# Kernel optimization log

Hardware: AMD Instinct MI355X
Metric: run time of the kernel (lower is better)

## Reference

```python
import jax, jax.numpy as jnp
import numpy as np

ALPHA = 0.25
GAMMA = 2.0
EPS = 1e-4


def calc_iou(a, b):
    # a: [A,4] anchors xyxy, b: [M,4] gt boxes xyxy -> [A,M]
    area = (b[:, 2] - b[:, 0]) * (b[:, 3] - b[:, 1])  # [M]
    iw = jnp.minimum(a[:, 2:3], b[None, :, 2]) - jnp.maximum(a[:, 0:1], b[None, :, 0])
    ih = jnp.minimum(a[:, 3:4], b[None, :, 3]) - jnp.maximum(a[:, 1:2], b[None, :, 1])
    iw = jnp.clip(iw, 0.0)
    ih = jnp.clip(ih, 0.0)
    anchor_area = ((a[:, 2] - a[:, 0]) * (a[:, 3] - a[:, 1]))[:, None]
    ua = jnp.clip(anchor_area + area[None, :] - iw * ih, 1e-8)
    return iw * ih / ua


def setup_inputs() -> dict:
    B, A, K, M = 8, 120000, 80, 32
    key = jax.random.key(0)
    k1, k2, k3, k4, k5, k6, k7 = jax.random.split(key, 7)
    classifications = jax.random.uniform(k1, (B, A, K), dtype=jnp.float32)
    regressions = jax.random.normal(k2, (B, A, 4), dtype=jnp.float32) * 0.1
    # anchors: valid xyxy boxes with positive width/height
    a_xy = jax.random.uniform(k3, (A, 2), minval=0.0, maxval=480.0)
    a_wh = jax.random.uniform(k4, (A, 2), minval=16.0, maxval=128.0)
    anchors = jnp.concatenate([a_xy, a_xy + a_wh], axis=1)[None].astype(jnp.float32)
    # annotations: [B, M, 5] valid gt boxes, labels in [0, K)
    g_xy = jax.random.uniform(k5, (B, M, 2), minval=0.0, maxval=400.0)
    g_wh = jax.random.uniform(k6, (B, M, 2), minval=20.0, maxval=120.0)
    labels = jax.random.randint(k7, (B, M, 1), 0, K).astype(jnp.float32)
    annotations = jnp.concatenate([g_xy, g_xy + g_wh, labels], axis=2).astype(jnp.float32)
    return {"classifications": classifications, "regressions": regressions,
            "anchors": anchors, "annotations": annotations}


def reference(classifications, regressions, anchors, annotations):
    anchor = anchors[0]  # [A,4]
    aw = anchor[:, 2] - anchor[:, 0]
    ah = anchor[:, 3] - anchor[:, 1]
    acx = anchor[:, 0] + 0.5 * aw
    acy = anchor[:, 1] + 0.5 * ah
    reg_scale = jnp.array([0.1, 0.1, 0.2, 0.2], dtype=classifications.dtype)

    def per_item(cls, reg, ann):
        # cls: [A,K], reg: [A,4], ann: [M,5]
        valid = ann[:, 4] != -1.0  # [M] padding mask
        c = jnp.clip(cls, EPS, 1.0 - EPS)
        iou = jnp.where(valid[None, :], calc_iou(anchor, ann[:, :4]), -1.0)  # [A,M]
        iou_max = iou.max(axis=1)
        iou_argmax = iou.argmax(axis=1)
        assigned = ann[iou_argmax]  # [A,5] gather
        pos = iou_max >= 0.5
        neg = iou_max < 0.4
        num_pos = pos.sum().astype(c.dtype)
        # targets: 1 at assigned class for positives, 0 for negatives, -1 = ignore
        onehot = jax.nn.one_hot(assigned[:, 4].astype(jnp.int32), c.shape[1], dtype=c.dtype)
        t = jnp.where(pos[:, None], onehot, jnp.where(neg[:, None], 0.0, -1.0))
        alpha_factor = jnp.where(t == 1.0, ALPHA, 1.0 - ALPHA)
        focal_weight = jnp.where(t == 1.0, 1.0 - c, c)
        bce = -(t * jnp.log(c) + (1.0 - t) * jnp.log(1.0 - c))
        cls_loss = jnp.where(t != -1.0, alpha_factor * focal_weight ** GAMMA * bce, 0.0)
        cls_loss = cls_loss.sum() / jnp.maximum(num_pos, 1.0)
        gw0 = assigned[:, 2] - assigned[:, 0]
        gh0 = assigned[:, 3] - assigned[:, 1]
        gcx = assigned[:, 0] + 0.5 * gw0
        gcy = assigned[:, 1] + 0.5 * gh0
        gw = jnp.maximum(gw0, 1.0)
        gh = jnp.maximum(gh0, 1.0)
        rt = jnp.stack([(gcx - acx) / aw, (gcy - acy) / ah,
                        jnp.log(gw / aw), jnp.log(gh / ah)], axis=1) / reg_scale
        diff = jnp.abs(rt - reg)
        smooth = jnp.where(diff <= 1.0 / 9.0, 0.5 * 9.0 * diff ** 2, diff - 0.5 / 9.0)
        reg_loss = jnp.where(num_pos > 0.0,
                             (smooth * pos[:, None]).sum() / jnp.maximum(num_pos * 4.0, 1.0),
                             0.0)
        return cls_loss, reg_loss

    cls_l, reg_l = jax.vmap(per_item)(classifications, regressions, annotations)
    return cls_l.mean(keepdims=True), reg_l.mean(keepdims=True)
```

## Files before the change

kernel.cpp:

```cpp
#include <hip/hip_runtime.h>

#define NB 8
#define NA 120000
#define NK 80
#define NM 32

#define ALPHA_F 0.25f
#define EPS_F 1e-4f

#define BLK 256
#define BPB ((NA + BLK - 1) / BLK)

__device__ __forceinline__ float clampc(float x) {
    return fminf(fmaxf(x, EPS_F), 1.0f - EPS_F);
}
__device__ __forceinline__ float negl(float c) {
    return (1.0f - ALPHA_F) * c * c * (-__logf(1.0f - c));
}
__device__ __forceinline__ float posl(float c) {
    const float omc = 1.0f - c;
    return ALPHA_F * omc * omc * (-__logf(c));
}
__device__ __forceinline__ float negl4(float4 v) {
    return negl(clampc(v.x)) + negl(clampc(v.y)) + negl(clampc(v.z)) + negl(clampc(v.w));
}

__global__ __launch_bounds__(BLK) void fused_kernel(
    const float* __restrict__ anchors,
    const float* __restrict__ regressions,
    const float* __restrict__ annotations,
    const float* __restrict__ cls,
    float* __restrict__ part)
{
    const int b = blockIdx.x / BPB;
    const int blk = blockIdx.x % BPB;
    const int a0 = blk * BLK;
    const int a = a0 + threadIdx.x;

    __shared__ float ann[NM * 5];
    __shared__ float barea[NM];
    __shared__ int s_ign[BLK];
    __shared__ int s_nign;
    if (threadIdx.x == 0) s_nign = 0;
    if (threadIdx.x < NM * 5) ann[threadIdx.x] = annotations[b * NM * 5 + threadIdx.x];
    __syncthreads();
    if (threadIdx.x < NM) {
        const float* r = &ann[threadIdx.x * 5];
        barea[threadIdx.x] = (r[2] - r[0]) * (r[3] - r[1]);
    }
    __syncthreads();

    float reg_local = 0.0f;
    float pos_local = 0.0f;
    float cls_local = 0.0f;

    if (a < NA) {
        const float4 av = ((const float4*)anchors)[a];
        const float aw = av.z - av.x;
        const float ah = av.w - av.y;
        const float aarea = aw * ah;

        float bi = -1.0f, bu = 1.0f;
        int bm = 0;
        #pragma unroll
        for (int m = 0; m < NM; ++m) {
            const float bx1 = ann[m * 5 + 0];
            const float by1 = ann[m * 5 + 1];
            const float bx2 = ann[m * 5 + 2];
            const float by2 = ann[m * 5 + 3];
            const float lbl = ann[m * 5 + 4];
            const float iw = fmaxf(fminf(av.z, bx2) - fmaxf(av.x, bx1), 0.0f);
            const float ih = fmaxf(fminf(av.w, by2) - fmaxf(av.y, by1), 0.0f);
            float inter = iw * ih;
            float ua = fmaxf(aarea + barea[m] - inter, 1e-8f);
            if (lbl == -1.0f) { inter = -1.0f; ua = 1.0f; }
            if (m == 0 || inter * bu > bi * ua) { bi = inter; bu = ua; bm = m; }
        }

        if (bi >= 0.5f * bu) {
            const int st = (int)ann[bm * 5 + 4];
            const float bx1 = ann[bm * 5 + 0];
            const float by1 = ann[bm * 5 + 1];
            const float bx2 = ann[bm * 5 + 2];
            const float by2 = ann[bm * 5 + 3];
            const float gw0 = bx2 - bx1;
            const float gh0 = by2 - by1;
            const float gcx = bx1 + 0.5f * gw0;
            const float gcy = by1 + 0.5f * gh0;
            const float gw = fmaxf(gw0, 1.0f);
            const float gh = fmaxf(gh0, 1.0f);
            const float acx = av.x + 0.5f * aw;
            const float acy = av.y + 0.5f * ah;
            const float rt0 = ((gcx - acx) / aw) / 0.1f;
            const float rt1 = ((gcy - acy) / ah) / 0.1f;
            const float rt2 = logf(gw / aw) / 0.2f;
            const float rt3 = logf(gh / ah) / 0.2f;
            const float4 rg = ((const float4*)regressions)[b * NA + a];
            float s = 0.0f, d;
            d = fabsf(rt0 - rg.x); s += (d <= 1.0f / 9.0f) ? 4.5f * d * d : d - 0.5f / 9.0f;
            d = fabsf(rt1 - rg.y); s += (d <= 1.0f / 9.0f) ? 4.5f * d * d : d - 0.5f / 9.0f;
            d = fabsf(rt2 - rg.z); s += (d <= 1.0f / 9.0f) ? 4.5f * d * d : d - 0.5f / 9.0f;
            d = fabsf(rt3 - rg.w); s += (d <= 1.0f / 9.0f) ? 4.5f * d * d : d - 0.5f / 9.0f;
            reg_local = s;
            pos_local = 1.0f;
            const float c = clampc(cls[((size_t)b * NA + a) * NK + st]);
            cls_local = posl(c) - negl(c);
        } else if (bi >= 0.4f * bu) {
            const int k = atomicAdd(&s_nign, 1);
            s_ign[k] = threadIdx.x;
        }
    }
    __syncthreads();

    const float4* __restrict__ p = (const float4*)(cls + ((size_t)b * NA + a0) * NK);
    const int n_rows = (a0 + BLK <= NA) ? BLK : (NA - a0);

    if (n_rows == BLK) {
        #pragma unroll
        for (int o = 0; o < 4; ++o) {
            float4 v[5];
            #pragma unroll
            for (int u = 0; u < 5; ++u)
                v[u] = p[(o * 5 + u) * BLK + threadIdx.x];
            #pragma unroll
            for (int u = 0; u < 5; ++u)
                cls_local += negl4(v[u]);
        }
    } else {
        const int n4 = n_rows * 20;
        for (int idx = threadIdx.x; idx < n4; idx += BLK)
            cls_local += negl4(p[idx]);
    }

    const int nign = s_nign;
    if (nign > 0) {
        const int total = nign * 20;
        for (int i = threadIdx.x; i < total; i += BLK) {
            const int e = i / 20;
            const int f = i - e * 20;
            const int r = s_ign[e];
            cls_local -= negl4(p[r * 20 + f]);
        }
    }

    #pragma unroll
    for (int o = 32; o > 0; o >>= 1) {
        cls_local += __shfl_down(cls_local, o, 64);
        reg_local += __shfl_down(reg_local, o, 64);
        pos_local += __shfl_down(pos_local, o, 64);
    }
    __shared__ float wc[BLK / 64], wr[BLK / 64], wp[BLK / 64];
    const int lane = threadIdx.x & 63;
    const int wid = threadIdx.x >> 6;
    if (lane == 0) { wc[wid] = cls_local; wr[wid] = reg_local; wp[wid] = pos_local; }
    __syncthreads();
    if (threadIdx.x == 0) {
        float csum = 0.0f, rsum = 0.0f, psum = 0.0f;
        #pragma unroll
        for (int i = 0; i < BLK / 64; ++i) { csum += wc[i]; rsum += wr[i]; psum += wp[i]; }
        float4 q;
        q.x = csum; q.y = rsum; q.z = psum; q.w = 0.0f;
        ((float4*)part)[blockIdx.x] = q;
    }
}

__global__ __launch_bounds__(256) void finalize_kernel(
    const float* __restrict__ part,
    float* __restrict__ out)
{
    __shared__ float red[3][4];
    float cs_total = 0.0f, rs_total = 0.0f;
    for (int b = 0; b < NB; ++b) {
        float c = 0.0f, r = 0.0f, p = 0.0f;
        for (int i = threadIdx.x; i < BPB; i += 256) {
            const float4 q = ((const float4*)part)[b * BPB + i];
            c += q.x; r += q.y; p += q.z;
        }
        #pragma unroll
        for (int o = 32; o > 0; o >>= 1) {
            c += __shfl_down(c, o, 64);
            r += __shfl_down(r, o, 64);
            p += __shfl_down(p, o, 64);
        }
        const int lane = threadIdx.x & 63;
        const int wid = threadIdx.x >> 6;
        if (lane == 0) { red[0][wid] = c; red[1][wid] = r; red[2][wid] = p; }
        __syncthreads();
        if (threadIdx.x == 0) {
            const float C = red[0][0] + red[0][1] + red[0][2] + red[0][3];
            const float R = red[1][0] + red[1][1] + red[1][2] + red[1][3];
            const float P = red[2][0] + red[2][1] + red[2][2] + red[2][3];
            cs_total += C / fmaxf(P, 1.0f);
            rs_total += (P > 0.0f) ? R / fmaxf(P * 4.0f, 1.0f) : 0.0f;
        }
        __syncthreads();
    }
    if (threadIdx.x == 0) {
        out[0] = cs_total / (float)NB;
        out[1] = rs_total / (float)NB;
    }
}

extern "C" void kernel_launch(void* const* d_in, const int* in_sizes, int n_in,
                              void* d_out, int out_size, void* d_ws, size_t ws_size,
                              hipStream_t stream) {
    const float* cls = (const float*)d_in[0];
    const float* reg = (const float*)d_in[1];
    const float* anc = (const float*)d_in[2];
    const float* ann = (const float*)d_in[3];

    float* part = (float*)d_ws;
    float* out = (float*)d_out;

    fused_kernel<<<NB * BPB, BLK, 0, stream>>>(anc, reg, ann, cls, part);
    finalize_kernel<<<1, 256, 0, stream>>>(part, out);
}
```

Before: 83.54 us.

## Prefetch classification tiles before IoU matching and parallelize finalize per batch

```diff
diff --git a/kernel.cpp b/kernel.cpp
--- a/kernel.cpp
+++ b/kernel.cpp
@@ -10,6 +10,7 @@
 
 #define BLK 256
 #define BPB ((NA + BLK - 1) / BLK)
+
 
 __device__ __forceinline__ float clampc(float x) {
     return fminf(fmaxf(x, EPS_F), 1.0f - EPS_F);
@@ -49,6 +50,19 @@
         barea[threadIdx.x] = (r[2] - r[0]) * (r[3] - r[1]);
     }
     __syncthreads();
+
+    const float4* __restrict__ p = (const float4*)(cls + ((size_t)b * NA + a0) * NK);
+    const float4* __restrict__ q = p + threadIdx.x;
+    const int n_rows = (a0 + BLK <= NA) ? BLK : (NA - a0);
+    const bool full = (n_rows == BLK);
+
+    float4 A[5], B[5];
+    if (full) {
+        #pragma unroll
+        for (int u = 0; u < 5; ++u) A[u] = q[u * BLK];
+        #pragma unroll
+        for (int u = 0; u < 5; ++u) B[u] = q[(5 + u) * BLK];
+    }
 
     float reg_local = 0.0f;
     float pos_local = 0.0f;
@@ -112,20 +126,21 @@
     }
     __syncthreads();
 
-    const float4* __restrict__ p = (const float4*)(cls + ((size_t)b * NA + a0) * NK);
-    const int n_rows = (a0 + BLK <= NA) ? BLK : (NA - a0);
-
-    if (n_rows == BLK) {
-        #pragma unroll
-        for (int o = 0; o < 4; ++o) {
-            float4 v[5];
-            #pragma unroll
-            for (int u = 0; u < 5; ++u)
-                v[u] = p[(o * 5 + u) * BLK + threadIdx.x];
-            #pragma unroll
-            for (int u = 0; u < 5; ++u)
-                cls_local += negl4(v[u]);
-        }
+    if (full) {
+        float s = 0.0f;
+        #pragma unroll
+        for (int u = 0; u < 5; ++u) s += negl4(A[u]);
+        #pragma unroll
+        for (int u = 0; u < 5; ++u) A[u] = q[(10 + u) * BLK];
+        #pragma unroll
+        for (int u = 0; u < 5; ++u) s += negl4(B[u]);
+        #pragma unroll
+        for (int u = 0; u < 5; ++u) B[u] = q[(15 + u) * BLK];
+        #pragma unroll
+        for (int u = 0; u < 5; ++u) s += negl4(A[u]);
+        #pragma unroll
+        for (int u = 0; u < 5; ++u) s += negl4(B[u]);
+        cls_local += s;
     } else {
         const int n4 = n_rows * 20;
         for (int idx = threadIdx.x; idx < n4; idx += BLK)
@@ -158,46 +173,43 @@
         float csum = 0.0f, rsum = 0.0f, psum = 0.0f;
         #pragma unroll
         for (int i = 0; i < BLK / 64; ++i) { csum += wc[i]; rsum += wr[i]; psum += wp[i]; }
-        float4 q;
-        q.x = csum; q.y = rsum; q.z = psum; q.w = 0.0f;
-        ((float4*)part)[blockIdx.x] = q;
-    }
-}
-
-__global__ __launch_bounds__(256) void finalize_kernel(
+        float4 o4;
+        o4.x = csum; o4.y = rsum; o4.z = psum; o4.w = 0.0f;
+        ((float4*)part)[blockIdx.x] = o4;
+    }
+}
+
+__global__ __launch_bounds__(512) void finalize_kernel(
     const float* __restrict__ part,
     float* __restrict__ out)
 {
-    __shared__ float red[3][4];
-    float cs_total = 0.0f, rs_total = 0.0f;
-    for (int b = 0; b < NB; ++b) {
-        float c = 0.0f, r = 0.0f, p = 0.0f;
-        for (int i = threadIdx.x; i < BPB; i += 256) {
-            const float4 q = ((const float4*)part)[b * BPB + i];
-            c += q.x; r += q.y; p += q.z;
-        }
-        #pragma unroll
-        for (int o = 32; o > 0; o >>= 1) {
-            c += __shfl_down(c, o, 64);
-            r += __shfl_down(r, o, 64);
-            p += __shfl_down(p, o, 64);
-        }
-        const int lane = threadIdx.x & 63;
-        const int wid = threadIdx.x >> 6;
-        if (lane == 0) { red[0][wid] = c; red[1][wid] = r; red[2][wid] = p; }
-        __syncthreads();
-        if (threadIdx.x == 0) {
-            const float C = red[0][0] + red[0][1] + red[0][2] + red[0][3];
-            const float R = red[1][0] + red[1][1] + red[1][2] + red[1][3];
-            const float P = red[2][0] + red[2][1] + red[2][2] + red[2][3];
-            cs_total += C / fmaxf(P, 1.0f);
-            rs_total += (P > 0.0f) ? R / fmaxf(P * 4.0f, 1.0f) : 0.0f;
-        }
-        __syncthreads();
-    }
+    __shared__ float redC[NB], redR[NB], redP[NB];
+    const int w = threadIdx.x >> 6;
+    const int lane = threadIdx.x & 63;
+
+    float c = 0.0f, r = 0.0f, p = 0.0f;
+    for (int i = lane; i < BPB; i += 64) {
+        const float4 q = ((const float4*)part)[w * BPB + i];
+        c += q.x; r += q.y; p += q.z;
+    }
+    #pragma unroll
+    for (int o = 32; o > 0; o >>= 1) {
+        c += __shfl_down(c, o, 64);
+        r += __shfl_down(r, o, 64);
+        p += __shfl_down(p, o, 64);
+    }
+    if (lane == 0) { redC[w] = c; redR[w] = r; redP[w] = p; }
+    __syncthreads();
     if (threadIdx.x == 0) {
-        out[0] = cs_total / (float)NB;
-        out[1] = rs_total / (float)NB;
+        float cs = 0.0f, rs = 0.0f;
+        #pragma unroll
+        for (int b = 0; b < NB; ++b) {
+            const float P = redP[b];
+            cs += redC[b] / fmaxf(P, 1.0f);
+            rs += (P > 0.0f) ? redR[b] / fmaxf(P * 4.0f, 1.0f) : 0.0f;
+        }
+        out[0] = cs / (float)NB;
+        out[1] = rs / (float)NB;
     }
 }
 
@@ -213,5 +225,5 @@
     float* out = (float*)d_out;
 
     fused_kernel<<<NB * BPB, BLK, 0, stream>>>(anc, reg, ann, cls, part);
-    finalize_kernel<<<1, 256, 0, stream>>>(part, out);
-}
+    finalize_kernel<<<1, 512, 0, stream>>>(part, out);
+}
```

Result: slower. 102.2 us (+22.4%).
